# Optimization experiments

Hardware: AMD Instinct MI355X
Metric: run time of the kernel (lower is better)

## Reference

```python
import jax, jax.numpy as jnp
import numpy as np

N_NODES = 50000
N_EDGES = 600000
N_GRAPHS = 2500
F_IN = 11  # QM9 num_node_features


def setup_inputs() -> dict:
    key = jax.random.key(0)
    ks = jax.random.split(key, 14)
    x = jax.random.normal(ks[0], (N_NODES, F_IN), jnp.float32)
    edge_index = jax.random.randint(ks[1], (2, N_EDGES), 0, N_NODES)
    batch = jnp.sort(jax.random.randint(ks[2], (N_NODES,), 0, N_GRAPHS))

    def lin(k, fan_in, fan_out):
        s = 1.0 / np.sqrt(fan_in)
        return jax.random.uniform(k, (fan_in, fan_out), jnp.float32, -s, s)

    params = dict(
        W1=lin(ks[3], F_IN, 128), b1=jnp.zeros((128,), jnp.float32),
        W2=lin(ks[4], 128, 64),   b2=jnp.zeros((64,), jnp.float32),
        Wf1=lin(ks[5], 64, 128),  bf1=jnp.zeros((128,), jnp.float32),
        Wf2=lin(ks[6], 128, 64),  bf2=jnp.zeros((64,), jnp.float32),
        Wf3=lin(ks[7], 64, 1),    bf3=jnp.zeros((1,), jnp.float32),
    )
    return dict(x=x, edge_index=edge_index, batch=batch, **params)


def reference(x, edge_index, batch, W1, b1, W2, b2, Wf1, bf1, Wf2, bf2, Wf3, bf3):
    N = x.shape[0]
    # --- GCN normalization (PyG gcn_norm): add self-loops, symmetric D^-1/2 A D^-1/2 ---
    self_loop = jnp.arange(N)
    src = jnp.concatenate([edge_index[0], self_loop])  # [E+N]
    dst = jnp.concatenate([edge_index[1], self_loop])
    deg = jax.ops.segment_sum(jnp.ones_like(dst, jnp.float32), dst, num_segments=N)
    dis = jnp.where(deg > 0, jax.lax.rsqrt(jnp.maximum(deg, 1.0)), 0.0)  # deg^-1/2
    norm = dis[src] * dis[dst]  # [E+N]

    def gcn_conv(h, W, b):
        h = h @ W  # transform first (small fan-in)
        msg = h[src] * norm[:, None]  # gather + normalize
        return jax.ops.segment_sum(msg, dst, num_segments=N) + b  # scatter-add

    h = jax.nn.relu(gcn_conv(x, W1, b1))
    h = jax.nn.relu(gcn_conv(h, W2, b2))

    # --- global_mean_pool ---
    sums = jax.ops.segment_sum(h, batch, num_segments=N_GRAPHS)
    cnt = jax.ops.segment_sum(jnp.ones((N,), jnp.float32), batch, num_segments=N_GRAPHS)
    g = sums / jnp.maximum(cnt, 1.0)[:, None]  # [G, 64]

    # --- MLP head ---
    g = jax.nn.relu(g @ Wf1 + bf1)
    g = jax.nn.relu(g @ Wf2 + bf2)
    return g @ Wf3 + bf3  # [G, 1]
```

## Files before the change

kernel.cpp:

```cpp
#include <hip/hip_runtime.h>

#define F0 11
#define F1 128
#define F2 64

__global__ void k_count(const int* __restrict__ dst, int E, int* __restrict__ cnt) {
    int e = blockIdx.x * blockDim.x + threadIdx.x;
    if (e < E) atomicAdd(&cnt[dst[e]], 1);
}

__global__ void k_scanA(const int* __restrict__ deg, int* __restrict__ rowloc,
                        int* __restrict__ bsum, int N) {
    __shared__ int s[256];
    int i = blockIdx.x * 256 + threadIdx.x;
    int v = (i < N) ? deg[i] : 0;
    s[threadIdx.x] = v;
    __syncthreads();
    for (int o = 1; o < 256; o <<= 1) {
        int t = (threadIdx.x >= o) ? s[threadIdx.x - o] : 0;
        __syncthreads();
        s[threadIdx.x] += t;
        __syncthreads();
    }
    if (i < N) rowloc[i] = s[threadIdx.x] - v;
    if (threadIdx.x == 255) bsum[blockIdx.x] = s[255];
}

__global__ void k_scanB(int* __restrict__ bsum, int B) {
    __shared__ int s[256];
    int t = threadIdx.x;
    int v = (t < B) ? bsum[t] : 0;
    s[t] = v;
    __syncthreads();
    for (int o = 1; o < 256; o <<= 1) {
        int u = (t >= o) ? s[t - o] : 0;
        __syncthreads();
        s[t] += u;
        __syncthreads();
    }
    if (t < B) bsum[t] = s[t] - v;
}

__global__ void k_scanC(const int* __restrict__ rowloc, const int* __restrict__ bsum,
                        const int* __restrict__ deg, int* __restrict__ rowptr,
                        int* __restrict__ cursor, float* __restrict__ dis, int N) {
    int i = blockIdx.x * 256 + threadIdx.x;
    if (i < N) {
        int r = rowloc[i] + bsum[blockIdx.x];
        rowptr[i] = r;
        cursor[i] = r;
        dis[i] = 1.0f / sqrtf((float)(deg[i] + 1));
    }
}

__global__ void k_scatter(const int* __restrict__ src, const int* __restrict__ dst,
                          const float* __restrict__ dis, int* __restrict__ cursor,
                          int2* __restrict__ epack, int E) {
    int e = blockIdx.x * blockDim.x + threadIdx.x;
    if (e >= E) return;
    int s = src[e], d = dst[e];
    int pos = atomicAdd(&cursor[d], 1);
    epack[pos] = make_int2(s, __float_as_int(dis[s]));
}

__global__ void k_agg1l1(const int* __restrict__ rowptr, const int* __restrict__ deg,
                         const int2* __restrict__ epack, const float* __restrict__ x,
                         const float* __restrict__ dis, const float* __restrict__ W1,
                         const float* __restrict__ b1, float* __restrict__ h1, int N) {
    __shared__ float sW[F0 * F1];
    __shared__ float sb[F1];
    int t = threadIdx.x;
    for (int i = t; i < F0 * F1; i += 256) sW[i] = W1[i];
    if (t < F1) sb[t] = b1[t];
    __syncthreads();

    int wid = t >> 6, lane = t & 63;
    int n = blockIdx.x * 4 + wid;
    if (n >= N) return;

    int r0 = rowptr[n], r1 = r0 + deg[n];
    int eo = lane >> 4, f = lane & 15;

    float acc = 0.0f;
    int j = r0 + eo;
    for (; j + 4 < r1; j += 8) {
        int2 p = epack[j];
        int2 q = epack[j + 4];
        if (f < F0) {
            acc += x[p.x * F0 + f] * __int_as_float(p.y);
            acc += x[q.x * F0 + f] * __int_as_float(q.y);
        }
    }
    if (j < r1) {
        int2 p = epack[j];
        if (f < F0) acc += x[p.x * F0 + f] * __int_as_float(p.y);
    }
    acc += __shfl_xor(acc, 16, 64);
    acc += __shfl_xor(acc, 32, 64);

    float dn = dis[n];
    float afull = acc * dn;
    if (f < F0) afull += x[n * F0 + f] * dn * dn;

    float o1 = sb[lane], o2 = sb[lane + 64];
#pragma unroll
    for (int k = 0; k < F0; k++) {
        float ak = __shfl(afull, k, 64);
        o1 += ak * sW[k * F1 + lane];
        o2 += ak * sW[k * F1 + lane + 64];
    }
    h1[(size_t)n * F1 + lane]      = fmaxf(o1, 0.0f);
    h1[(size_t)n * F1 + lane + 64] = fmaxf(o2, 0.0f);
}

__global__ void k_l2(const float* __restrict__ h1, const float* __restrict__ W2,
                     float* __restrict__ t2, int N) {
    __shared__ float sW[F1 * F2];
    __shared__ float sh[4][F1];
    int t = threadIdx.x;
    int grp = t >> 6, lane = t & 63;
    for (int i = t; i < F1 * F2; i += 256) sW[i] = W2[i];
    int n0 = blockIdx.x * 16;
    for (int r = 0; r < 4; r++) {
        int n = n0 + r * 4 + grp;
        __syncthreads();
        if (n < N) {
            sh[grp][lane]      = h1[(size_t)n * F1 + lane];
            sh[grp][lane + 64] = h1[(size_t)n * F1 + lane + 64];
        }
        __syncthreads();
        if (n < N) {
            float acc = 0.0f;
#pragma unroll
            for (int k = 0; k < F1; k++) acc += sh[grp][k] * sW[k * F2 + lane];
            t2[(size_t)n * F2 + lane] = acc;
        }
    }
}

__global__ void k_agg2pool(const int* __restrict__ rowptr, const int* __restrict__ deg,
                           const int2* __restrict__ epack, const float* __restrict__ t2,
                           const float* __restrict__ dis, const float* __restrict__ b2,
                           const int* __restrict__ batch, float* __restrict__ gsum,
                           float* __restrict__ gcnt, int N) {
    int t = threadIdx.x;
    int wid = t >> 6, lane = t & 63;
    int n = blockIdx.x * 4 + wid;
    if (n >= N) return;

    int r0 = rowptr[n], r1 = r0 + deg[n];
    float a0 = 0.f, a1 = 0.f, a2 = 0.f, a3 = 0.f;
    int j = r0;
    if (r1 - r0 >= 4) {
        int2 p0 = epack[j], p1 = epack[j + 1], p2 = epack[j + 2], p3 = epack[j + 3];
        j += 4;
        while (j + 4 <= r1) {
            int2 q0 = epack[j], q1 = epack[j + 1], q2 = epack[j + 2], q3 = epack[j + 3];
            a0 += __int_as_float(p0.y) * t2[(size_t)p0.x * F2 + lane];
            a1 += __int_as_float(p1.y) * t2[(size_t)p1.x * F2 + lane];
            a2 += __int_as_float(p2.y) * t2[(size_t)p2.x * F2 + lane];
            a3 += __int_as_float(p3.y) * t2[(size_t)p3.x * F2 + lane];
            p0 = q0; p1 = q1; p2 = q2; p3 = q3;
            j += 4;
        }
        a0 += __int_as_float(p0.y) * t2[(size_t)p0.x * F2 + lane];
        a1 += __int_as_float(p1.y) * t2[(size_t)p1.x * F2 + lane];
        a2 += __int_as_float(p2.y) * t2[(size_t)p2.x * F2 + lane];
        a3 += __int_as_float(p3.y) * t2[(size_t)p3.x * F2 + lane];
    }
    for (; j < r1; j++) {
        int2 p = epack[j];
        a0 += __int_as_float(p.y) * t2[(size_t)p.x * F2 + lane];
    }
    float acc = (a0 + a1) + (a2 + a3);
    float dn = dis[n];
    float h2 = fmaxf(acc * dn + t2[(size_t)n * F2 + lane] * dn * dn + b2[lane], 0.0f);
    int g = batch[n];
    atomicAdd(&gsum[(size_t)g * F2 + lane], h2);
    if (lane == 0) atomicAdd(&gcnt[g], 1.0f);
}

__global__ void k_head(const float* __restrict__ gsum, const float* __restrict__ gcnt,
                       const float* __restrict__ Wf1, const float* __restrict__ bf1,
                       const float* __restrict__ Wf2, const float* __restrict__ bf2,
                       const float* __restrict__ Wf3, const float* __restrict__ bf3,
                       float* __restrict__ out, int G) {
    __shared__ float sg[F2];
    __shared__ float sh1[F1];
    __shared__ float sh2[F2];
    int g = blockIdx.x, t = threadIdx.x;
    if (t < F2) {
        float c = fmaxf(gcnt[g], 1.0f);
        sg[t] = gsum[g * F2 + t] / c;
    }
    __syncthreads();
    {
        float a = bf1[t];
#pragma unroll 8
        for (int k = 0; k < F2; k++) a += sg[k] * Wf1[k * F1 + t];
        sh1[t] = fmaxf(a, 0.0f);
    }
    __syncthreads();
    if (t < F2) {
        float a = bf2[t];
#pragma unroll 8
        for (int k = 0; k < F1; k++) a += sh1[k] * Wf2[k * F2 + t];
        sh2[t] = fmaxf(a, 0.0f);
    }
    __syncthreads();
    if (t < F2) {
        float v = sh2[t] * Wf3[t];
        for (int off = 32; off > 0; off >>= 1) v += __shfl_down(v, off, 64);
        if (t == 0) out[g] = v + bf3[0];
    }
}

extern "C" void kernel_launch(void* const* d_in, const int* in_sizes, int n_in,
                              void* d_out, int out_size, void* d_ws, size_t ws_size,
                              hipStream_t stream) {
    const float* x     = (const float*)d_in[0];
    const int*   ei    = (const int*)d_in[1];
    const int*   batch = (const int*)d_in[2];
    const float* W1    = (const float*)d_in[3];
    const float* b1    = (const float*)d_in[4];
    const float* W2    = (const float*)d_in[5];
    const float* b2    = (const float*)d_in[6];
    const float* Wf1   = (const float*)d_in[7];
    const float* bf1   = (const float*)d_in[8];
    const float* Wf2   = (const float*)d_in[9];
    const float* bf2   = (const float*)d_in[10];
    const float* Wf3   = (const float*)d_in[11];
    const float* bf3   = (const float*)d_in[12];
    float* out = (float*)d_out;

    const int N = in_sizes[0] / F0;
    const int E = in_sizes[1] / 2;
    const int G = out_size;
    const int* src = ei;
    const int* dst = ei + E;

    size_t off = 0;
    auto carve = [&](size_t bytes) {
        void* p = (char*)d_ws + off;
        off += (bytes + 255) & ~(size_t)255;
        return p;
    };
    int*   deg    = (int*)  carve((size_t)N * 4);
    int*   rowloc = (int*)  carve((size_t)N * 4);
    int*   rowptr = (int*)  carve((size_t)N * 4);
    int*   cursor = (int*)  carve((size_t)N * 4);
    int*   bsum   = (int*)  carve(256 * 4);
    float* dis    = (float*)carve((size_t)N * 4);
    int2*  epack  = (int2*) carve((size_t)E * 8);
    float* h1     = (float*)carve((size_t)N * F1 * 4);
    float* t2     = (float*)carve((size_t)N * F2 * 4);
    float* gsum   = (float*)carve((size_t)G * (F2 + 1) * 4);
    float* gcnt   = gsum + (size_t)G * F2;
    (void)ws_size; (void)n_in;

    const int NB = (N + 255) / 256;

    hipMemsetAsync(deg,  0, (size_t)N * 4, stream);
    hipMemsetAsync(gsum, 0, (size_t)G * (F2 + 1) * 4, stream);

    k_count  <<<(E + 255) / 256, 256, 0, stream>>>(dst, E, deg);
    k_scanA  <<<NB, 256, 0, stream>>>(deg, rowloc, bsum, N);
    k_scanB  <<<1, 256, 0, stream>>>(bsum, NB);
    k_scanC  <<<NB, 256, 0, stream>>>(rowloc, bsum, deg, rowptr, cursor, dis, N);
    k_scatter<<<(E + 255) / 256, 256, 0, stream>>>(src, dst, dis, cursor, epack, E);
    k_agg1l1 <<<(N + 3) / 4, 256, 0, stream>>>(rowptr, deg, epack, x, dis, W1, b1, h1, N);
    k_l2     <<<(N + 15) / 16, 256, 0, stream>>>(h1, W2, t2, N);
    k_agg2pool<<<(N + 3) / 4, 256, 0, stream>>>(rowptr, deg, epack, t2, dis, b2, batch, gsum, gcnt, N);
    k_head   <<<G, F1, 0, stream>>>(gsum, gcnt, Wf1, bf1, Wf2, bf2, Wf3, bf3, out, G);
}
```

Before: 287.1 us.

## Split layer-2 features into 16-wide column chunks aggregated in four passes

Layer-2 output t2 is now stored column-chunked (four slabs of N x 16), and the aggregation+pool kernel runs four times, once per feature chunk. Inside each pass a wavefront handles four edges at once (four 16-lane slots) and reduces across slots with shuffles. The intent is that each pass gathers from a 3.2 MB slab that fits in cache, improving gather hit rates. The cost is reading the edge list and rowptr four times, four launches, and 64B gather granularity.

```diff
diff --git a/kernel.cpp b/kernel.cpp
--- a/kernel.cpp
+++ b/kernel.cpp
@@ -114,7 +114,7 @@
 }
 
 __global__ void k_l2(const float* __restrict__ h1, const float* __restrict__ W2,
-                     float* __restrict__ t2, int N) {
+                     float* __restrict__ t2c, int N) {
     __shared__ float sW[F1 * F2];
     __shared__ float sh[4][F1];
     int t = threadIdx.x;
@@ -133,51 +133,44 @@
             float acc = 0.0f;
 #pragma unroll
             for (int k = 0; k < F1; k++) acc += sh[grp][k] * sW[k * F2 + lane];
-            t2[(size_t)n * F2 + lane] = acc;
+            t2c[((size_t)(lane >> 4) * N + n) * 16 + (lane & 15)] = acc;
         }
     }
 }
 
-__global__ void k_agg2pool(const int* __restrict__ rowptr, const int* __restrict__ deg,
-                           const int2* __restrict__ epack, const float* __restrict__ t2,
-                           const float* __restrict__ dis, const float* __restrict__ b2,
-                           const int* __restrict__ batch, float* __restrict__ gsum,
-                           float* __restrict__ gcnt, int N) {
+__global__ void k_agg2pool_c(const int* __restrict__ rowptr, const int* __restrict__ deg,
+                             const int2* __restrict__ epack, const float* __restrict__ t2c,
+                             const float* __restrict__ dis, const float* __restrict__ b2,
+                             const int* __restrict__ batch, float* __restrict__ gsum,
+                             float* __restrict__ gcnt, int N, int pass) {
     int t = threadIdx.x;
     int wid = t >> 6, lane = t & 63;
     int n = blockIdx.x * 4 + wid;
     if (n >= N) return;
+    int slot = lane >> 4, f = lane & 15;
+    const float* __restrict__ chunk = t2c + (size_t)pass * N * 16;
 
     int r0 = rowptr[n], r1 = r0 + deg[n];
-    float a0 = 0.f, a1 = 0.f, a2 = 0.f, a3 = 0.f;
-    int j = r0;
-    if (r1 - r0 >= 4) {
-        int2 p0 = epack[j], p1 = epack[j + 1], p2 = epack[j + 2], p3 = epack[j + 3];
-        j += 4;
-        while (j + 4 <= r1) {
-            int2 q0 = epack[j], q1 = epack[j + 1], q2 = epack[j + 2], q3 = epack[j + 3];
-            a0 += __int_as_float(p0.y) * t2[(size_t)p0.x * F2 + lane];
-            a1 += __int_as_float(p1.y) * t2[(size_t)p1.x * F2 + lane];
-            a2 += __int_as_float(p2.y) * t2[(size_t)p2.x * F2 + lane];
-            a3 += __int_as_float(p3.y) * t2[(size_t)p3.x * F2 + lane];
-            p0 = q0; p1 = q1; p2 = q2; p3 = q3;
-            j += 4;
-        }
-        a0 += __int_as_float(p0.y) * t2[(size_t)p0.x * F2 + lane];
-        a1 += __int_as_float(p1.y) * t2[(size_t)p1.x * F2 + lane];
-        a2 += __int_as_float(p2.y) * t2[(size_t)p2.x * F2 + lane];
-        a3 += __int_as_float(p3.y) * t2[(size_t)p3.x * F2 + lane];
-    }
-    for (; j < r1; j++) {
-        int2 p = epack[j];
-        a0 += __int_as_float(p.y) * t2[(size_t)p.x * F2 + lane];
-    }
-    float acc = (a0 + a1) + (a2 + a3);
+    float acc = 0.0f;
+    int j = r0 + slot;
+    for (; j + 4 < r1; j += 8) {
+        int2 p = epack[j];
+        int2 q = epack[j + 4];
+        acc += __int_as_float(p.y) * chunk[p.x * 16 + f];
+        acc += __int_as_float(q.y) * chunk[q.x * 16 + f];
+    }
+    if (j < r1) {
+        int2 p = epack[j];
+        acc += __int_as_float(p.y) * chunk[p.x * 16 + f];
+    }
+    acc += __shfl_xor(acc, 16, 64);
+    acc += __shfl_xor(acc, 32, 64);
+
     float dn = dis[n];
-    float h2 = fmaxf(acc * dn + t2[(size_t)n * F2 + lane] * dn * dn + b2[lane], 0.0f);
+    float h2 = fmaxf(acc * dn + chunk[n * 16 + f] * dn * dn + b2[pass * 16 + f], 0.0f);
     int g = batch[n];
-    atomicAdd(&gsum[(size_t)g * F2 + lane], h2);
-    if (lane == 0) atomicAdd(&gcnt[g], 1.0f);
+    if (slot == 0) atomicAdd(&gsum[(size_t)g * F2 + pass * 16 + f], h2);
+    if (lane == 0 && pass == 0) atomicAdd(&gcnt[g], 1.0f);
 }
 
 __global__ void k_head(const float* __restrict__ gsum, const float* __restrict__ gcnt,
@@ -253,7 +246,7 @@
     float* dis    = (float*)carve((size_t)N * 4);
     int2*  epack  = (int2*) carve((size_t)E * 8);
     float* h1     = (float*)carve((size_t)N * F1 * 4);
-    float* t2     = (float*)carve((size_t)N * F2 * 4);
+    float* t2c    = (float*)carve((size_t)N * F2 * 4);
     float* gsum   = (float*)carve((size_t)G * (F2 + 1) * 4);
     float* gcnt   = gsum + (size_t)G * F2;
     (void)ws_size; (void)n_in;
@@ -269,7 +262,9 @@
     k_scanC  <<<NB, 256, 0, stream>>>(rowloc, bsum, deg, rowptr, cursor, dis, N);
     k_scatter<<<(E + 255) / 256, 256, 0, stream>>>(src, dst, dis, cursor, epack, E);
     k_agg1l1 <<<(N + 3) / 4, 256, 0, stream>>>(rowptr, deg, epack, x, dis, W1, b1, h1, N);
-    k_l2     <<<(N + 15) / 16, 256, 0, stream>>>(h1, W2, t2, N);
-    k_agg2pool<<<(N + 3) / 4, 256, 0, stream>>>(rowptr, deg, epack, t2, dis, b2, batch, gsum, gcnt, N);
+    k_l2     <<<(N + 15) / 16, 256, 0, stream>>>(h1, W2, t2c, N);
+    for (int p = 0; p < 4; p++)
+        k_agg2pool_c<<<(N + 3) / 4, 256, 0, stream>>>(rowptr, deg, epack, t2c, dis, b2,
+                                                      batch, gsum, gcnt, N, p);
     k_head   <<<G, F1, 0, stream>>>(gsum, gcnt, Wf1, bf1, Wf2, bf2, Wf3, bf3, out, G);
 }
```

Result: slower. 343.2 us (+19.5%).

## Register-tile the second-layer dense transform with 4x4 outer-product blocking

Applied to the files above, without the earlier changes.

Replaces the per-node matrix-vector k_l2 kernel with a tiled GEMM kernel that processes 64 nodes per block. The h1 tile is loaded with float4 reads and stored transposed in shared memory, and each thread computes a 4x4 output tile from vectorized shared-memory loads. Each block loads W2 once for 64 nodes instead of 16, and the redundant syncs of the old loop are gone. Shared memory use grows to about 66KB per block, which may limit occupancy. The transposed writes into shared memory may also cause bank conflicts.

```diff
diff --git a/kernel.cpp b/kernel.cpp
--- a/kernel.cpp
+++ b/kernel.cpp
@@ -3,6 +3,7 @@
 #define F0 11
 #define F1 128
 #define F2 64
+#define TN 64
 
 __global__ void k_count(const int* __restrict__ dst, int E, int* __restrict__ cnt) {
     int e = blockIdx.x * blockDim.x + threadIdx.x;
@@ -113,29 +114,43 @@
     h1[(size_t)n * F1 + lane + 64] = fmaxf(o2, 0.0f);
 }
 
-__global__ void k_l2(const float* __restrict__ h1, const float* __restrict__ W2,
-                     float* __restrict__ t2, int N) {
+__global__ __launch_bounds__(256)
+void k_l2gemm(const float* __restrict__ h1, const float* __restrict__ W2,
+              float* __restrict__ t2, int N) {
     __shared__ float sW[F1 * F2];
-    __shared__ float sh[4][F1];
-    int t = threadIdx.x;
-    int grp = t >> 6, lane = t & 63;
-    for (int i = t; i < F1 * F2; i += 256) sW[i] = W2[i];
-    int n0 = blockIdx.x * 16;
-    for (int r = 0; r < 4; r++) {
-        int n = n0 + r * 4 + grp;
-        __syncthreads();
-        if (n < N) {
-            sh[grp][lane]      = h1[(size_t)n * F1 + lane];
-            sh[grp][lane + 64] = h1[(size_t)n * F1 + lane + 64];
-        }
-        __syncthreads();
-        if (n < N) {
-            float acc = 0.0f;
-#pragma unroll
-            for (int k = 0; k < F1; k++) acc += sh[grp][k] * sW[k * F2 + lane];
-            t2[(size_t)n * F2 + lane] = acc;
-        }
-    }
+    __shared__ float sHt[F1][TN + 4];
+    int t = threadIdx.x;
+    for (int idx = t; idx < F1 * F2 / 4; idx += 256)
+        ((float4*)sW)[idx] = ((const float4*)W2)[idx];
+    int n0 = blockIdx.x * TN;
+    int nn = min(TN, N - n0);
+    for (int idx = t; idx < nn * (F1 / 4); idx += 256) {
+        int r = idx >> 5;
+        int q = idx & 31;
+        float4 v = ((const float4*)(h1 + (size_t)(n0 + r) * F1))[q];
+        sHt[4 * q + 0][r] = v.x;
+        sHt[4 * q + 1][r] = v.y;
+        sHt[4 * q + 2][r] = v.z;
+        sHt[4 * q + 3][r] = v.w;
+    }
+    __syncthreads();
+
+    int i = t >> 4, j = t & 15;
+    float4 c0 = {0,0,0,0}, c1 = {0,0,0,0}, c2 = {0,0,0,0}, c3 = {0,0,0,0};
+#pragma unroll 4
+    for (int k = 0; k < F1; k++) {
+        float4 b = ((const float4*)(sW + k * F2))[j];
+        float4 a = *(const float4*)&sHt[k][4 * i];
+        c0.x += a.x * b.x; c0.y += a.x * b.y; c0.z += a.x * b.z; c0.w += a.x * b.w;
+        c1.x += a.y * b.x; c1.y += a.y * b.y; c1.z += a.y * b.z; c1.w += a.y * b.w;
+        c2.x += a.z * b.x; c2.y += a.z * b.y; c2.z += a.z * b.z; c2.w += a.z * b.w;
+        c3.x += a.w * b.x; c3.y += a.w * b.y; c3.z += a.w * b.z; c3.w += a.w * b.w;
+    }
+    int nb = n0 + 4 * i;
+    if (nb + 0 < N) ((float4*)(t2 + (size_t)(nb + 0) * F2))[j] = c0;
+    if (nb + 1 < N) ((float4*)(t2 + (size_t)(nb + 1) * F2))[j] = c1;
+    if (nb + 2 < N) ((float4*)(t2 + (size_t)(nb + 2) * F2))[j] = c2;
+    if (nb + 3 < N) ((float4*)(t2 + (size_t)(nb + 3) * F2))[j] = c3;
 }
 
 __global__ void k_agg2pool(const int* __restrict__ rowptr, const int* __restrict__ deg,
@@ -269,7 +284,7 @@
     k_scanC  <<<NB, 256, 0, stream>>>(rowloc, bsum, deg, rowptr, cursor, dis, N);
     k_scatter<<<(E + 255) / 256, 256, 0, stream>>>(src, dst, dis, cursor, epack, E);
     k_agg1l1 <<<(N + 3) / 4, 256, 0, stream>>>(rowptr, deg, epack, x, dis, W1, b1, h1, N);
-    k_l2     <<<(N + 15) / 16, 256, 0, stream>>>(h1, W2, t2, N);
+    k_l2gemm <<<(N + TN - 1) / TN, 256, 0, stream>>>(h1, W2, t2, N);
     k_agg2pool<<<(N + 3) / 4, 256, 0, stream>>>(rowptr, deg, epack, t2, dis, b2, batch, gsum, gcnt, N);
     k_head   <<<G, F1, 0, stream>>>(gsum, gcnt, Wf1, bf1, Wf2, bf2, Wf3, bf3, out, G);
 }
```

Measured after the change: 272.1 us. 1.06x faster.
